# Performance work log

Hardware: AMD Instinct MI355X
Metric: run time of the kernel (lower is better)

The kernel has to match this reference:

```python
import jax, jax.numpy as jnp
import numpy as np

N = 50000      # nodes
E = 800000     # edges (before self loops)
IN = 128       # in_channels
C = 64         # out_channels per head
H = 4          # heads (both layers)
NEG_SLOPE = 0.2


def setup_inputs():
    key = jax.random.key(0)
    ks = jax.random.split(key, 14)
    nrm = lambda k, sh, s: jax.random.normal(k, sh, dtype=jnp.float32) * s
    x = nrm(ks[0], (N, IN), 1.0)
    edge_index = jax.random.randint(ks[1], (2, E), 0, N, dtype=jnp.int32)
    batch = jnp.zeros((N,), dtype=jnp.int32)
    edge_attr = jax.random.uniform(ks[2], (E, 1), dtype=jnp.float32)
    # layer 1 params (PyG GATConv: lin, att_src, att_dst, lin_edge, att_edge, bias)
    W1 = nrm(ks[3], (IN, H * C), 1.0 / np.sqrt(IN))
    We1 = nrm(ks[4], (1, H * C), 1.0)
    att_s1 = nrm(ks[5], (H, C), 1.0 / np.sqrt(C))
    att_d1 = nrm(ks[6], (H, C), 1.0 / np.sqrt(C))
    att_e1 = nrm(ks[7], (H, C), 1.0 / np.sqrt(C))
    b1 = jnp.zeros((H * C,), dtype=jnp.float32)
    # layer 2 params (in = H*C = 256)
    W2 = nrm(ks[8], (H * C, H * C), 1.0 / np.sqrt(H * C))
    We2 = nrm(ks[9], (1, H * C), 1.0)
    att_s2 = nrm(ks[10], (H, C), 1.0 / np.sqrt(C))
    att_d2 = nrm(ks[11], (H, C), 1.0 / np.sqrt(C))
    att_e2 = nrm(ks[12], (H, C), 1.0 / np.sqrt(C))
    b2 = jnp.zeros((H * C,), dtype=jnp.float32)
    return dict(x=x, edge_index=edge_index, batch=batch, edge_attr=edge_attr,
                W1=W1, We1=We1, att_s1=att_s1, att_d1=att_d1, att_e1=att_e1, b1=b1,
                W2=W2, We2=We2, att_s2=att_s2, att_d2=att_d2, att_e2=att_e2, b2=b2)


def gat_layer(h_in, src, dst, e_attr, W, We, att_s, att_d, att_e, b):
    n = h_in.shape[0]
    h = (h_in @ W).reshape(n, H, C)                      # [N,H,C]
    a_src = jnp.einsum('nhc,hc->nh', h, att_s)           # [N,H]
    a_dst = jnp.einsum('nhc,hc->nh', h, att_d)
    e = (e_attr @ We).reshape(-1, H, C)                  # [E',H,C]
    a_edge = jnp.einsum('ehc,hc->eh', e, att_e)          # [E',H]
    alpha = jax.nn.leaky_relu(a_src[src] + a_dst[dst] + a_edge, NEG_SLOPE)
    # softmax over edges grouped by destination node
    amax = jax.ops.segment_max(alpha, dst, num_segments=n)
    amax = jnp.where(jnp.isfinite(amax), amax, 0.0)
    ex = jnp.exp(alpha - amax[dst])
    denom = jax.ops.segment_sum(ex, dst, num_segments=n)
    a = ex / (denom[dst] + 1e-16)                        # [E',H]
    out = jax.ops.segment_sum(a[:, :, None] * h[src], dst, num_segments=n)
    return out.reshape(n, H * C) + b


def reference(x, edge_index, batch, edge_attr,
              W1, We1, att_s1, att_d1, att_e1, b1,
              W2, We2, att_s2, att_d2, att_e2, b2):
    n = x.shape[0]
    # PyG GATConv default: add self loops, self-loop edge_attr = mean fill
    loop = jnp.arange(n, dtype=edge_index.dtype)
    src = jnp.concatenate([edge_index[0], loop])
    dst = jnp.concatenate([edge_index[1], loop])
    ea_fill = jnp.broadcast_to(edge_attr.mean(axis=0, keepdims=True), (n, edge_attr.shape[1]))
    ea = jnp.concatenate([edge_attr, ea_fill], axis=0)
    h1 = gat_layer(x, src, dst, ea, W1, We1, att_s1, att_d1, att_e1, b1)
    h2 = gat_layer(h1, src, dst, ea, W2, We2, att_s2, att_d2, att_e2, b2)
    return h2
```

## Files before the change

kernel.cpp:

```cpp
#include <hip/hip_runtime.h>

#define NEG_SLOPE 0.2f

typedef __attribute__((ext_vector_type(8))) short bf16x8;
typedef __attribute__((ext_vector_type(4))) float f32x4;

__device__ inline unsigned short f2bf(float x) {
  unsigned int u = __float_as_uint(x);
  u += 0x7fffu + ((u >> 16) & 1u);
  return (unsigned short)(u >> 16);
}

__device__ inline unsigned fkey(float x) {
  unsigned u = __float_as_uint(x);
  return (u >> 31) ? ~u : (u | 0x80000000u);
}
__device__ inline float fkey_dec(unsigned k) {
  unsigned u = (k & 0x80000000u) ? (k ^ 0x80000000u) : ~k;
  return __uint_as_float(u);
}


__global__ void hist_kernel(const int* __restrict__ ei, int* __restrict__ counts,
                            int E, int Etot) {
  int e = blockIdx.x * blockDim.x + threadIdx.x;
  if (e >= Etot) return;
  int d = (e < E) ? ei[E + e] : (e - E);
  atomicAdd(&counts[d], 1);
}

__global__ void mean_kernel(const float* __restrict__ ea, float* __restrict__ acc, int E) {
  int i = blockIdx.x * blockDim.x + threadIdx.x;
  float s = 0.f;
  for (; i < E; i += gridDim.x * blockDim.x) s += ea[i];
#pragma unroll
  for (int off = 1; off < 64; off <<= 1) s += __shfl_xor(s, off, 64);
  if ((threadIdx.x & 63) == 0) atomicAdd(acc, s);
}

__global__ void scan_blocksum(const int* __restrict__ counts, int* __restrict__ bsum, int Nn) {
  int base = blockIdx.x * 4096 + threadIdx.x * 16;
  int s = 0;
#pragma unroll
  for (int i = 0; i < 16; i++) { int idx = base + i; if (idx < Nn) s += counts[idx]; }
#pragma unroll
  for (int off = 1; off < 64; off <<= 1) s += __shfl_xor(s, off, 64);
  __shared__ int ws_[4];
  if ((threadIdx.x & 63) == 0) ws_[threadIdx.x >> 6] = s;
  __syncthreads();
  if (threadIdx.x == 0) bsum[blockIdx.x] = ws_[0] + ws_[1] + ws_[2] + ws_[3];
}

__global__ void scan_offsets(int* bsum, int nb, int* rowptrN,
                             const float* meanacc, float* meanv, int E) {
  if (threadIdx.x == 0 && blockIdx.x == 0) {
    int acc = 0;
    for (int i = 0; i < nb; i++) { int v = bsum[i]; bsum[i] = acc; acc += v; }
    *rowptrN = acc;
    *meanv = *meanacc / (float)E;
  }
}

__global__ void scan_final(const int* __restrict__ counts, const int* __restrict__ bsum,
                           int* __restrict__ rowptr, int* __restrict__ cursor, int Nn) {
  int base = blockIdx.x * 4096 + threadIdx.x * 16;
  int v[16]; int s = 0;
#pragma unroll
  for (int i = 0; i < 16; i++) { int idx = base + i; v[i] = (idx < Nn) ? counts[idx] : 0; s += v[i]; }
  int lane = threadIdx.x & 63, wv = threadIdx.x >> 6;
  int incl = s;
#pragma unroll
  for (int off = 1; off < 64; off <<= 1) {
    int y = __shfl_up(incl, off, 64);
    if (lane >= off) incl += y;
  }
  __shared__ int wtot[4];
  if (lane == 63) wtot[wv] = incl;
  __syncthreads();
  int run = bsum[blockIdx.x] + incl - s;
  for (int i = 0; i < wv; i++) run += wtot[i];
  for (int i = 0; i < 16; i++) {
    int idx = base + i;
    if (idx < Nn) { rowptr[idx] = run; cursor[idx] = run; }
    run += v[i];
  }
}

__global__ void scatter_kernel(const int* __restrict__ ei, const float* __restrict__ eattr,
                               const float* __restrict__ meanv,
                               int* __restrict__ cursor, int2* __restrict__ epack,
                               int E, int Etot) {
  int e = blockIdx.x * blockDim.x + threadIdx.x;
  if (e >= Etot) return;
  int d, s; float ea;
  if (e < E) { d = ei[E + e]; s = ei[e]; ea = eattr[e]; }
  else       { d = e - E;     s = e - E; ea = meanv[0]; }
  int pos = atomicAdd(&cursor[d], 1);
  epack[pos] = make_int2(s, __float_as_int(ea));
}

__global__ void weatt_kernel(const float* __restrict__ We1, const float* __restrict__ atte1,
                             const float* __restrict__ We2, const float* __restrict__ atte2,
                             float* __restrict__ weatt1, float* __restrict__ weatt2) {
  int t = threadIdx.x;
  const float* We = (t < 256) ? We1 : We2;
  const float* at = (t < 256) ? atte1 : atte2;
  float* wo = (t < 256) ? weatt1 : weatt2;
  int i = t & 255;
  float p = We[i] * at[i];
#pragma unroll
  for (int off = 1; off < 64; off <<= 1) p += __shfl_xor(p, off, 64);
  if ((i & 63) == 0) wo[i >> 6] = p;
}

__global__ void wtrans_kernel(const float* __restrict__ W1, unsigned short* __restrict__ Wt1,
                              const float* __restrict__ W2, unsigned short* __restrict__ Wt2) {
  int b = blockIdx.x;
  const float* W; unsigned short* Wt; int K, t;
  if (b < 128) { W = W1; Wt = Wt1; K = 128; t = b * 256 + threadIdx.x; }
  else         { W = W2; Wt = Wt2; K = 256; t = (b - 128) * 256 + threadIdx.x; }
  int n = t & 255, k = t >> 8;
  if (k >= K) return;
  Wt[(size_t)n * K + k] = f2bf(W[(size_t)k * 256 + n]);
}


#define CS_STRIDE 264

template <int AF32>
__global__ __launch_bounds__(512) void gemm_att(const void* __restrict__ Ain,
                                                const unsigned short* __restrict__ Wt,
                                                unsigned short* __restrict__ Hb,
                                                const float* __restrict__ atts,
                                                const float* __restrict__ attd,
                                                float* __restrict__ asrc,
                                                float* __restrict__ adst,
                                                unsigned* __restrict__ gmaxk,
                                                int M, int K) {
  __shared__ __align__(16) short smem[128 * CS_STRIDE];
  short* As = smem;
  short* Bs = smem + 128 * 64;
  short* Cs = smem;
  const int tid = threadIdx.x;
  const int lane = tid & 63, wv = tid >> 6;
  const int wm = wv >> 2, wn = wv & 3;
  const int l15 = lane & 15, l4 = lane >> 4;
  const int bm = blockIdx.x * 128;

  f32x4 acc[4][4] = {};

  for (int k0 = 0; k0 < K; k0 += 64) {
    {
      int r0 = tid >> 3, kc = (tid & 7) * 8;
#pragma unroll
      for (int rr = 0; rr < 2; rr++) {
        int r = r0 + rr * 64;
        int gr = bm + r;
        bf16x8 v = {};
        if (gr < M) {
          if (AF32) {
            const float* src = (const float*)Ain + (size_t)gr * K + k0 + kc;
            float4 f0 = *(const float4*)src;
            float4 f1 = *(const float4*)(src + 4);
            v[0] = (short)f2bf(f0.x); v[1] = (short)f2bf(f0.y);
            v[2] = (short)f2bf(f0.z); v[3] = (short)f2bf(f0.w);
            v[4] = (short)f2bf(f1.x); v[5] = (short)f2bf(f1.y);
            v[6] = (short)f2bf(f1.z); v[7] = (short)f2bf(f1.w);
          } else {
            v = *(const bf16x8*)((const unsigned short*)Ain + (size_t)gr * K + k0 + kc);
          }
        }
        *(bf16x8*)&As[(r * 64 + kc) ^ ((r & 7) << 3)] = v;
      }
    }
    {
      int c = tid & 7, nb = tid >> 3;
#pragma unroll
      for (int it = 0; it < 4; it++) {
        int n = nb + 64 * it;
        bf16x8 v = *(const bf16x8*)&Wt[(size_t)n * K + k0 + c * 8];
        *(bf16x8*)&Bs[(n * 64 + c * 8) ^ ((n & 7) << 3)] = v;
      }
    }
    __syncthreads();
    bf16x8 af[4][2], bfr[4][2];
#pragma unroll
    for (int rt = 0; rt < 4; rt++)
#pragma unroll
      for (int ks = 0; ks < 2; ks++) {
        int row = wm * 64 + rt * 16 + l15;
        int kb = l4 * 8 + ks * 32;
        af[rt][ks] = *(const bf16x8*)&As[(row * 64 + kb) ^ ((row & 7) << 3)];
      }
#pragma unroll
    for (int ct = 0; ct < 4; ct++)
#pragma unroll
      for (int ks = 0; ks < 2; ks++) {
        int n = wn * 64 + ct * 16 + l15;
        int kb = l4 * 8 + ks * 32;
        bfr[ct][ks] = *(const bf16x8*)&Bs[(n * 64 + kb) ^ ((n & 7) << 3)];
      }
#pragma unroll
    for (int rt = 0; rt < 4; rt++)
#pragma unroll
      for (int ct = 0; ct < 4; ct++)
#pragma unroll
        for (int ks = 0; ks < 2; ks++)
          acc[rt][ct] = __builtin_amdgcn_mfma_f32_16x16x32_bf16(
              af[rt][ks], bfr[ct][ks], acc[rt][ct], 0, 0, 0);
    __syncthreads();
  }

  float s_att[4], d_att[4];
#pragma unroll
  for (int ct = 0; ct < 4; ct++) {
    s_att[ct] = atts[wn * 64 + ct * 16 + l15];
    d_att[ct] = attd[wn * 64 + ct * 16 + l15];
  }
  float ps[4][4] = {}, pd[4][4] = {};
#pragma unroll
  for (int rt = 0; rt < 4; rt++)
#pragma unroll
    for (int ct = 0; ct < 4; ct++)
#pragma unroll
      for (int i = 0; i < 4; i++) {
        float v = acc[rt][ct][i];
        int row = wm * 64 + rt * 16 + l4 * 4 + i;
        Cs[row * CS_STRIDE + wn * 64 + ct * 16 + l15] = f2bf(v);
        ps[rt][i] = fmaf(v, s_att[ct], ps[rt][i]);
        pd[rt][i] = fmaf(v, d_att[ct], pd[rt][i]);
      }
  __syncthreads();

  {
    int row = tid >> 2, seg = tid & 3;
    int gr = bm + row;
    if (gr < M) {
      const short* srcr = &Cs[row * CS_STRIDE + seg * 64];
      unsigned short* dstr = &Hb[(size_t)gr * 256 + seg * 64];
#pragma unroll
      for (int k = 0; k < 8; k++)
        *(uint4*)&dstr[k * 8] = *(const uint4*)&srcr[k * 8];
    }
  }

#pragma unroll
  for (int rt = 0; rt < 4; rt++)
#pragma unroll
    for (int i = 0; i < 4; i++) {
#pragma unroll
      for (int off = 1; off < 16; off <<= 1) {
        ps[rt][i] += __shfl_xor(ps[rt][i], off, 64);
        pd[rt][i] += __shfl_xor(pd[rt][i], off, 64);
      }
    }
  float mx = ps[0][0];
#pragma unroll
  for (int rt = 0; rt < 4; rt++)
#pragma unroll
    for (int i = 0; i < 4; i++) mx = fmaxf(mx, ps[rt][i]);
  mx = fmaxf(mx, __shfl_xor(mx, 16, 64));
  mx = fmaxf(mx, __shfl_xor(mx, 32, 64));
  if (lane == 0) atomicMax(&gmaxk[wn * 32], fkey(mx));
  if (l15 == 0) {
#pragma unroll
    for (int rt = 0; rt < 4; rt++)
#pragma unroll
      for (int i = 0; i < 4; i++) {
        int gr = bm + wm * 64 + rt * 16 + l4 * 4 + i;
        if (gr < M) {
          asrc[gr * 4 + wn] = ps[rt][i];
          adst[gr * 4 + wn] = pd[rt][i];
        }
      }
  }
}


#define AGG_PH1(CNT)                                                        \
  int src = 0; float w = 0.f;                                               \
  if (il < (CNT)) {                                                         \
    int2 e = epack[p + il];                                                 \
    float al = fmaf(__int_as_float(e.y), wa, asrc[e.x * 4 + hh] + ad);      \
    al = fmaxf(al, NEG_SLOPE * al);                                         \
    w = __expf(al - b);                                                     \
    src = e.x;                                                              \
  }                                                                         \
  ssum += w;

#define AGG_GATHER(i)                                                       \
  {                                                                         \
    int sl = (i) | hb16;                                                    \
    int si = __shfl(src, sl, 64);                                           \
    float wi = __shfl(w, sl, 64);                                           \
    uint2 hv = *(const uint2*)&Hb[(size_t)((unsigned)si * 256u + co)];      \
    acc.x = fmaf(wi, __uint_as_float(hv.x << 16), acc.x);                   \
    acc.y = fmaf(wi, __uint_as_float(hv.x & 0xffff0000u), acc.y);           \
    acc.z = fmaf(wi, __uint_as_float(hv.y << 16), acc.z);                   \
    acc.w = fmaf(wi, __uint_as_float(hv.y & 0xffff0000u), acc.w);           \
  }

template <int OUTBF>
__global__ __launch_bounds__(256) void gat_agg(const unsigned short* __restrict__ Hb,
                                               const float* __restrict__ asrc,
                                               const float* __restrict__ adst,
                                               const int* __restrict__ rowptr,
                                               const int2* __restrict__ epack,
                                               const float* __restrict__ weatt,
                                               const unsigned* __restrict__ gmaxk,
                                               const float* __restrict__ bias,
                                               unsigned short* __restrict__ outb,
                                               float* __restrict__ outf, int Nn) {
  int wid = (blockIdx.x * blockDim.x + threadIdx.x) >> 6;
  int lane = threadIdx.x & 63;
  if (wid >= Nn) return;
  int beg = rowptr[wid], end = rowptr[wid + 1];
  int hh = lane >> 4;
  int il = lane & 15;
  int hb16 = lane & 48;
  float wa = weatt[hh];
  float ad = adst[wid * 4 + hh];
  float braw = ad + fkey_dec(gmaxk[hh * 32]) + fmaxf(wa, 0.f);
  float b = fmaxf(braw, NEG_SLOPE * braw);
  unsigned co = (unsigned)lane * 4u;

  float ssum = 0.f;
  float4 acc = {0.f, 0.f, 0.f, 0.f};

  int p = beg;
  for (; p + 16 <= end; p += 16) {
    AGG_PH1(16)
#pragma unroll
    for (int i = 0; i < 16; i++) AGG_GATHER(i)
  }
  int cnt = end - p;
  if (cnt > 0) {
    AGG_PH1(cnt)
    for (int i = 0; i < cnt; i++) AGG_GATHER(i)
  }

#pragma unroll
  for (int off = 1; off < 16; off <<= 1) ssum += __shfl_xor(ssum, off, 64);

  float inv = 1.f / (ssum + 1e-16f);
  float4 b4 = *(const float4*)&bias[co];
  float4 r;
  r.x = fmaf(acc.x, inv, b4.x);
  r.y = fmaf(acc.y, inv, b4.y);
  r.z = fmaf(acc.z, inv, b4.z);
  r.w = fmaf(acc.w, inv, b4.w);
  if (OUTBF) {
    unsigned lo = (unsigned)f2bf(r.x) | ((unsigned)f2bf(r.y) << 16);
    unsigned hi = (unsigned)f2bf(r.z) | ((unsigned)f2bf(r.w) << 16);
    *(uint2*)&outb[(size_t)wid * 256 + co] = make_uint2(lo, hi);
  } else {
    *(float4*)&outf[(size_t)wid * 256 + co] = r;
  }
}


extern "C" void kernel_launch(void* const* d_in, const int* in_sizes, int n_in,
                              void* d_out, int out_size, void* d_ws, size_t ws_size,
                              hipStream_t stream) {
  (void)n_in; (void)out_size; (void)ws_size;
  const float* x     = (const float*)d_in[0];
  const int*   ei    = (const int*)d_in[1];
  const float* eattr = (const float*)d_in[3];
  const float* W1    = (const float*)d_in[4];
  const float* We1   = (const float*)d_in[5];
  const float* atts1 = (const float*)d_in[6];
  const float* attd1 = (const float*)d_in[7];
  const float* atte1 = (const float*)d_in[8];
  const float* b1    = (const float*)d_in[9];
  const float* W2    = (const float*)d_in[10];
  const float* We2   = (const float*)d_in[11];
  const float* atts2 = (const float*)d_in[12];
  const float* attd2 = (const float*)d_in[13];
  const float* atte2 = (const float*)d_in[14];
  const float* b2    = (const float*)d_in[15];
  float* out = (float*)d_out;

  const int Nn   = in_sizes[0] / 128;
  const int E    = in_sizes[1] / 2;
  const int Etot = E + Nn;

  char* p = (char*)d_ws;
  auto alloc = [&](size_t bytes) { void* r = (void*)p; p += (bytes + 255) & ~(size_t)255; return r; };
  int*      counts  = (int*)alloc((size_t)Nn * 4);
  float*    meanacc = (float*)alloc(4);
  unsigned* gmaxk1  = (unsigned*)alloc(512);
  unsigned* gmaxk2  = (unsigned*)alloc(512);
  char* zero_end = p;
  int*   rowptr  = (int*)alloc((size_t)(Nn + 1) * 4);
  int*   cursor  = (int*)alloc((size_t)Nn * 4);
  int2*  epack   = (int2*)alloc((size_t)Etot * 8);
  int*   bsum    = (int*)alloc(64 * 4);
  float* meanv   = (float*)alloc(4);
  float* weatt1  = (float*)alloc(16);
  float* weatt2  = (float*)alloc(16);
  float* asrc    = (float*)alloc((size_t)Nn * 4 * 4);
  float* adst    = (float*)alloc((size_t)Nn * 4 * 4);
  unsigned short* hbuf = (unsigned short*)alloc((size_t)Nn * 256 * 2);
  unsigned short* h1b  = (unsigned short*)alloc((size_t)Nn * 256 * 2);
  unsigned short* Wt1  = (unsigned short*)alloc((size_t)256 * 128 * 2);
  unsigned short* Wt2  = (unsigned short*)alloc((size_t)256 * 256 * 2);

  const int NB = (Nn + 4095) / 4096;

  hipMemsetAsync(counts, 0, (size_t)(zero_end - (char*)counts), stream);

  hist_kernel<<<(Etot + 255) / 256, 256, 0, stream>>>(ei, counts, E, Etot);
  mean_kernel<<<512, 256, 0, stream>>>(eattr, meanacc, E);
  scan_blocksum<<<NB, 256, 0, stream>>>(counts, bsum, Nn);
  scan_offsets<<<1, 64, 0, stream>>>(bsum, NB, rowptr + Nn, meanacc, meanv, E);
  scan_final<<<NB, 256, 0, stream>>>(counts, bsum, rowptr, cursor, Nn);
  scatter_kernel<<<(Etot + 255) / 256, 256, 0, stream>>>(ei, eattr, meanv, cursor, epack, E, Etot);
  weatt_kernel<<<1, 512, 0, stream>>>(We1, atte1, We2, atte2, weatt1, weatt2);
  wtrans_kernel<<<384, 256, 0, stream>>>(W1, Wt1, W2, Wt2);

  const int gemmBlocks = (Nn + 127) / 128;
  const int nodeBlocks = (Nn + 3) / 4;

  gemm_att<1><<<gemmBlocks, 512, 0, stream>>>(x, Wt1, hbuf, atts1, attd1,
                                              asrc, adst, gmaxk1, Nn, 128);
  gat_agg<1><<<nodeBlocks, 256, 0, stream>>>(hbuf, asrc, adst, rowptr, epack,
                                             weatt1, gmaxk1, b1, h1b, nullptr, Nn);
  gemm_att<0><<<gemmBlocks, 512, 0, stream>>>(h1b, Wt2, hbuf, atts2, attd2,
                                              asrc, adst, gmaxk2, Nn, 256);
  gat_agg<0><<<nodeBlocks, 256, 0, stream>>>(hbuf, asrc, adst, rowptr, epack,
                                             weatt2, gmaxk2, b2, nullptr, out, Nn);
}
```

Baseline: 344.4 us.

## Prefetch next K tile into registers and shrink GEMM LDS footprint

The GEMM main loop now issues global loads for the next K tile into registers right after the barrier, so they overlap with the MFMA work on the current tile, and stores them to LDS at the top of the next iteration. Shared memory is reduced from 128*264 to 384*64 shorts by writing the bf16 output tile in two 64-row halves through LDS. The smaller LDS allocation can allow more resident blocks per CU, at the cost of extra barriers in the epilogue and more registers held for the prefetch buffers.

```diff
diff --git a/kernel.cpp b/kernel.cpp
--- a/kernel.cpp
+++ b/kernel.cpp
@@ -125,6 +125,25 @@
 }
 
 
+template <int AF32>
+__device__ inline bf16x8 load_a_row(const void* Ain, int gr, int K, int kpos, int M) {
+  bf16x8 v = {};
+  if (gr < M) {
+    if (AF32) {
+      const float* src = (const float*)Ain + (size_t)gr * K + kpos;
+      float4 f0 = *(const float4*)src;
+      float4 f1 = *(const float4*)(src + 4);
+      v[0] = (short)f2bf(f0.x); v[1] = (short)f2bf(f0.y);
+      v[2] = (short)f2bf(f0.z); v[3] = (short)f2bf(f0.w);
+      v[4] = (short)f2bf(f1.x); v[5] = (short)f2bf(f1.y);
+      v[6] = (short)f2bf(f1.z); v[7] = (short)f2bf(f1.w);
+    } else {
+      v = *(const bf16x8*)((const unsigned short*)Ain + (size_t)gr * K + kpos);
+    }
+  }
+  return v;
+}
+
 #define CS_STRIDE 264
 
 template <int AF32>
@@ -137,7 +156,7 @@
                                                 float* __restrict__ adst,
                                                 unsigned* __restrict__ gmaxk,
                                                 int M, int K) {
-  __shared__ __align__(16) short smem[128 * CS_STRIDE];
+  __shared__ __align__(16) short smem[(128 + 256) * 64];
   short* As = smem;
   short* Bs = smem + 128 * 64;
   short* Cs = smem;
@@ -147,42 +166,37 @@
   const int l15 = lane & 15, l4 = lane >> 4;
   const int bm = blockIdx.x * 128;
 
+  const int r0 = tid >> 3, kc = (tid & 7) * 8;
+  const int nbB = tid >> 3, cB = (tid & 7) * 8;
+
   f32x4 acc[4][4] = {};
+  bf16x8 ra0, ra1, rb0, rb1, rb2, rb3;
+
+#define GLOAD_TILE(K0, A0, A1, B0, B1, B2, B3)                                 \
+  {                                                                            \
+    A0 = load_a_row<AF32>(Ain, bm + r0, K, (K0) + kc, M);                      \
+    A1 = load_a_row<AF32>(Ain, bm + r0 + 64, K, (K0) + kc, M);                 \
+    B0 = *(const bf16x8*)&Wt[(size_t)(nbB +   0) * K + (K0) + cB];             \
+    B1 = *(const bf16x8*)&Wt[(size_t)(nbB +  64) * K + (K0) + cB];             \
+    B2 = *(const bf16x8*)&Wt[(size_t)(nbB + 128) * K + (K0) + cB];             \
+    B3 = *(const bf16x8*)&Wt[(size_t)(nbB + 192) * K + (K0) + cB];             \
+  }
+
+  GLOAD_TILE(0, ra0, ra1, rb0, rb1, rb2, rb3)
 
   for (int k0 = 0; k0 < K; k0 += 64) {
-    {
-      int r0 = tid >> 3, kc = (tid & 7) * 8;
-#pragma unroll
-      for (int rr = 0; rr < 2; rr++) {
-        int r = r0 + rr * 64;
-        int gr = bm + r;
-        bf16x8 v = {};
-        if (gr < M) {
-          if (AF32) {
-            const float* src = (const float*)Ain + (size_t)gr * K + k0 + kc;
-            float4 f0 = *(const float4*)src;
-            float4 f1 = *(const float4*)(src + 4);
-            v[0] = (short)f2bf(f0.x); v[1] = (short)f2bf(f0.y);
-            v[2] = (short)f2bf(f0.z); v[3] = (short)f2bf(f0.w);
-            v[4] = (short)f2bf(f1.x); v[5] = (short)f2bf(f1.y);
-            v[6] = (short)f2bf(f1.z); v[7] = (short)f2bf(f1.w);
-          } else {
-            v = *(const bf16x8*)((const unsigned short*)Ain + (size_t)gr * K + k0 + kc);
-          }
-        }
-        *(bf16x8*)&As[(r * 64 + kc) ^ ((r & 7) << 3)] = v;
-      }
-    }
-    {
-      int c = tid & 7, nb = tid >> 3;
-#pragma unroll
-      for (int it = 0; it < 4; it++) {
-        int n = nb + 64 * it;
-        bf16x8 v = *(const bf16x8*)&Wt[(size_t)n * K + k0 + c * 8];
-        *(bf16x8*)&Bs[(n * 64 + c * 8) ^ ((n & 7) << 3)] = v;
-      }
-    }
+    *(bf16x8*)&As[((r0) * 64 + kc) ^ ((r0 & 7) << 3)] = ra0;
+    *(bf16x8*)&As[((r0 + 64) * 64 + kc) ^ ((r0 & 7) << 3)] = ra1;
+    *(bf16x8*)&Bs[((nbB) * 64 + cB) ^ ((nbB & 7) << 3)] = rb0;
+    *(bf16x8*)&Bs[((nbB + 64) * 64 + cB) ^ ((nbB & 7) << 3)] = rb1;
+    *(bf16x8*)&Bs[((nbB + 128) * 64 + cB) ^ ((nbB & 7) << 3)] = rb2;
+    *(bf16x8*)&Bs[((nbB + 192) * 64 + cB) ^ ((nbB & 7) << 3)] = rb3;
     __syncthreads();
+
+    bool more = (k0 + 64 < K);
+    bf16x8 na0, na1, nb0, nb1, nb2, nb3;
+    if (more) GLOAD_TILE(k0 + 64, na0, na1, nb0, nb1, nb2, nb3)
+
     bf16x8 af[4][2], bfr[4][2];
 #pragma unroll
     for (int rt = 0; rt < 4; rt++)
@@ -209,7 +223,10 @@
           acc[rt][ct] = __builtin_amdgcn_mfma_f32_16x16x32_bf16(
               af[rt][ks], bfr[ct][ks], acc[rt][ct], 0, 0, 0);
     __syncthreads();
-  }
+
+    if (more) { ra0 = na0; ra1 = na1; rb0 = nb0; rb1 = nb1; rb2 = nb2; rb3 = nb3; }
+  }
+#undef GLOAD_TILE
 
   float s_att[4], d_att[4];
 #pragma unroll
@@ -225,21 +242,31 @@
 #pragma unroll
       for (int i = 0; i < 4; i++) {
         float v = acc[rt][ct][i];
-        int row = wm * 64 + rt * 16 + l4 * 4 + i;
-        Cs[row * CS_STRIDE + wn * 64 + ct * 16 + l15] = f2bf(v);
         ps[rt][i] = fmaf(v, s_att[ct], ps[rt][i]);
         pd[rt][i] = fmaf(v, d_att[ct], pd[rt][i]);
       }
-  __syncthreads();
-
-  {
-    int row = tid >> 2, seg = tid & 3;
-    int gr = bm + row;
+
+  for (int h = 0; h < 2; h++) {
+    __syncthreads();
+    if (wm == h) {
+#pragma unroll
+      for (int rt = 0; rt < 4; rt++)
+#pragma unroll
+        for (int ct = 0; ct < 4; ct++)
+#pragma unroll
+          for (int i = 0; i < 4; i++) {
+            int lrow = rt * 16 + l4 * 4 + i;
+            Cs[lrow * CS_STRIDE + wn * 64 + ct * 16 + l15] = f2bf(acc[rt][ct][i]);
+          }
+    }
+    __syncthreads();
+    int row = tid >> 3, seg = tid & 7;
+    int gr = bm + h * 64 + row;
     if (gr < M) {
-      const short* srcr = &Cs[row * CS_STRIDE + seg * 64];
-      unsigned short* dstr = &Hb[(size_t)gr * 256 + seg * 64];
-#pragma unroll
-      for (int k = 0; k < 8; k++)
+      const short* srcr = &Cs[row * CS_STRIDE + seg * 32];
+      unsigned short* dstr = &Hb[(size_t)gr * 256 + seg * 32];
+#pragma unroll
+      for (int k = 0; k < 4; k++)
         *(uint4*)&dstr[k * 8] = *(const uint4*)&srcr[k * 8];
     }
   }
```

After: 344.3 us. Within noise of the previous version (-0.0%).
